# Performance work log

Measured on AMD Instinct MI355X. Metric: run time of the kernel, lower is better.

The kernel has to match this reference:

```python
import jax, jax.numpy as jnp
import numpy as np

DIM = 256
HEADS = 8
WIN = 8
HIDDEN = 1024
EPS = 1e-5

def _rel_pos_index(w):
    coords = np.stack(np.meshgrid(np.arange(w), np.arange(w), indexing='ij'))  # [2,w,w]
    cf = coords.reshape(2, -1)
    rel = cf[:, :, None] - cf[:, None, :]  # [2,N,N]
    rel = rel.transpose(1, 2, 0)
    rel[:, :, 0] += w - 1
    rel[:, :, 1] += w - 1
    rel[:, :, 0] *= 2 * w - 1
    return jnp.asarray(rel.sum(-1))  # [N,N] int

REL_IDX = _rel_pos_index(WIN)

def _layernorm(x, g, b):
    mu = jnp.mean(x, -1, keepdims=True)
    var = jnp.mean(jnp.square(x - mu), -1, keepdims=True)
    return (x - mu) * jax.lax.rsqrt(var + EPS) * g + b

def setup_inputs() -> dict:
    key = jax.random.key(0)
    ks = jax.random.split(key, 12)
    s = 0.02
    return {
        'x': jax.random.normal(ks[0], (16, 4096, 256), jnp.float32),
        'H': 64,
        'W': 64,
        'ln1_g': jnp.ones((DIM,), jnp.float32),
        'ln1_b': jnp.zeros((DIM,), jnp.float32),
        'qkv_w': jax.random.normal(ks[1], (DIM, 3 * DIM), jnp.float32) * s,
        'proj_w': jax.random.normal(ks[2], (DIM, DIM), jnp.float32) * s,
        'proj_b': jnp.zeros((DIM,), jnp.float32),
        'rel_bias_table': jax.random.normal(ks[3], ((2 * WIN - 1) ** 2, HEADS), jnp.float32) * s,
        'ln2_g': jnp.ones((DIM,), jnp.float32),
        'ln2_b': jnp.zeros((DIM,), jnp.float32),
        'fc1_w': jax.random.normal(ks[4], (DIM, HIDDEN), jnp.float32) * s,
        'fc1_b': jnp.zeros((HIDDEN,), jnp.float32),
        'fc2_w': jax.random.normal(ks[5], (HIDDEN, DIM), jnp.float32) * s,
        'fc2_b': jnp.zeros((DIM,), jnp.float32),
    }

def reference(x, H, W, ln1_g, ln1_b, qkv_w, proj_w, proj_b, rel_bias_table,
              ln2_g, ln2_b, fc1_w, fc1_b, fc2_w, fc2_b):
    B, L, C = x.shape
    w = WIN
    N = w * w
    head_dim = C // HEADS
    scale = head_dim ** -0.5

    shortcut = x
    h = _layernorm(x, ln1_g, ln1_b).reshape(B, H, W, C)
    # H, W chosen divisible by window_size -> pad_h = pad_w = 0 (faithful fast path)
    # window partition: [B*nW, N, C]
    h = h.reshape(B, H // w, w, W // w, w, C).transpose(0, 1, 3, 2, 4, 5)
    xw = h.reshape(-1, N, C)
    Bw = xw.shape[0]

    qkv = (xw @ qkv_w).reshape(Bw, N, 3, HEADS, head_dim)
    q = qkv[:, :, 0].transpose(0, 2, 1, 3) * scale  # [Bw,h,N,d]
    k = qkv[:, :, 1].transpose(0, 2, 1, 3)
    v = qkv[:, :, 2].transpose(0, 2, 1, 3)

    attn = jnp.einsum('bhnd,bhmd->bhnm', q, k)
    bias = rel_bias_table[REL_IDX.reshape(-1)].reshape(N, N, HEADS).transpose(2, 0, 1)
    attn = jax.nn.softmax(attn + bias[None], axis=-1)
    out = jnp.einsum('bhnm,bhmd->bhnd', attn, v).transpose(0, 2, 1, 3).reshape(Bw, N, C)
    out = out @ proj_w + proj_b

    # window reverse
    out = out.reshape(B, H // w, W // w, w, w, C).transpose(0, 1, 3, 2, 4, 5)
    out = out.reshape(B, L, C)

    x = shortcut + out
    h2 = _layernorm(x, ln2_g, ln2_b)
    mlp = jax.nn.gelu(h2 @ fc1_w + fc1_b, approximate=False) @ fc2_w + fc2_b
    return x + mlp
```

## Files before the change

kernel.cpp:

```cpp
#include <hip/hip_runtime.h>
#include <hip/hip_bf16.h>

typedef __attribute__((ext_vector_type(8))) short bf16x8;
typedef __attribute__((ext_vector_type(4))) float f32x4;

typedef __attribute__((address_space(3))) void LdsVoid;
typedef const __attribute__((address_space(1))) void GblVoid;

__device__ __forceinline__ void gload16(const void* g, void* l) {
  __builtin_amdgcn_global_load_lds((GblVoid*)g, (LdsVoid*)l, 16, 0, 0);
}

__device__ __forceinline__ unsigned short f2bf(float f) {
  union { float f; unsigned int u; } x; x.f = f;
  unsigned int r = (x.u + 0x7fffu + ((x.u >> 16) & 1u)) >> 16;
  return (unsigned short)r;
}

__global__ __launch_bounds__(256) void prep_w(
    const float* __restrict__ qw, const float* __restrict__ pw,
    const float* __restrict__ f1, const float* __restrict__ f2,
    unsigned short* __restrict__ out) {
  int idx = blockIdx.x * 256 + threadIdx.x;
  if (idx < 196608) { int n = idx >> 8, k = idx & 255; out[idx] = f2bf(qw[k * 768 + n]); return; }
  int i2 = idx - 196608;
  if (i2 < 65536) { int n = i2 >> 8, k = i2 & 255; out[idx] = f2bf(pw[k * 256 + n]); return; }
  int i3 = i2 - 65536;
  if (i3 < 262144) { int n = i3 >> 8, k = i3 & 255; out[idx] = f2bf(f1[k * 1024 + n]); return; }
  int i4 = i3 - 262144;
  { int n = i4 >> 10, k = i4 & 1023; out[idx] = f2bf(f2[k * 256 + n]); }
}

__global__ __launch_bounds__(256) void ln1_kernel(
    const float* __restrict__ x, const float* __restrict__ g, const float* __restrict__ b,
    unsigned short* __restrict__ xn) {
  int lane = threadIdx.x & 63, wid = threadIdx.x >> 6;
  size_t t = (size_t)blockIdx.x * 4 + wid;
  float4 v = ((const float4*)(x + t * 256))[lane];
  float s = v.x + v.y + v.z + v.w;
  #pragma unroll
  for (int m = 1; m < 64; m <<= 1) s += __shfl_xor(s, m);
  float mean = s * (1.0f / 256.0f);
  float dx = v.x - mean, dy = v.y - mean, dz = v.z - mean, dw = v.w - mean;
  float q = dx * dx + dy * dy + dz * dz + dw * dw;
  #pragma unroll
  for (int m = 1; m < 64; m <<= 1) q += __shfl_xor(q, m);
  float rstd = rsqrtf(q * (1.0f / 256.0f) + 1e-5f);
  float4 gg = ((const float4*)g)[lane];
  float4 bb = ((const float4*)b)[lane];
  unsigned int o0 = f2bf(dx * rstd * gg.x + bb.x) | ((unsigned int)f2bf(dy * rstd * gg.y + bb.y) << 16);
  unsigned int o1 = f2bf(dz * rstd * gg.z + bb.z) | ((unsigned int)f2bf(dw * rstd * gg.w + bb.w) << 16);
  int bI = (int)(t >> 12), rem = (int)t & 4095, y = rem >> 6, xc = rem & 63;
  size_t r = ((size_t)(bI * 64 + (y >> 3) * 8 + (xc >> 3))) * 64 + (y & 7) * 8 + (xc & 7);
  uint2 o; o.x = o0; o.y = o1;
  ((uint2*)(xn + r * 256))[lane] = o;
}

template <int EPI>
__global__ __launch_bounds__(256) void gemm_bt(
    const unsigned short* __restrict__ A, const unsigned short* __restrict__ Bt,
    unsigned short* __restrict__ outb, float* __restrict__ outf,
    const float* __restrict__ bias, int M, int N, int K) {
  __shared__ __align__(16) unsigned short lds_a[128 * 32];
  __shared__ __align__(16) unsigned short lds_b[128 * 32];
  const int tid = threadIdx.x;
  const int lane = tid & 63, wid = tid >> 6;
  const int cl = lane & 15, cg = lane >> 4;
  const size_t m0 = (size_t)blockIdx.y * 128;
  const size_t n0 = (size_t)blockIdx.x * 128;
  const int wr = wid >> 1, wc = wid & 1;
  f32x4 acc[4][4] = {};

  const unsigned short* aptr = A + (m0 + (tid >> 2)) * K + (tid & 3) * 8;
  const unsigned short* bptr = Bt + (n0 + (tid >> 2)) * K + (tid & 3) * 8;
  unsigned short* la = lds_a + wid * 512;
  unsigned short* lb = lds_b + wid * 512;
  const size_t astep = (size_t)64 * K;

  for (int k0 = 0; k0 < K; k0 += 32) {
    __syncthreads();
    gload16(aptr + k0, la);
    gload16(aptr + astep + k0, la + 2048);
    gload16(bptr + k0, lb);
    gload16(bptr + astep + k0, lb + 2048);
    __syncthreads();
    bf16x8 af[4], bfr[4];
    const unsigned short* pa = lds_a + (wr * 64 + cl) * 32 + cg * 8;
    const unsigned short* pb = lds_b + (wc * 64 + cl) * 32 + cg * 8;
    #pragma unroll
    for (int i = 0; i < 4; ++i) af[i] = *(const bf16x8*)(pa + i * 512);
    #pragma unroll
    for (int i = 0; i < 4; ++i) bfr[i] = *(const bf16x8*)(pb + i * 512);
    #pragma unroll
    for (int mi = 0; mi < 4; ++mi)
      #pragma unroll
      for (int ni = 0; ni < 4; ++ni)
        acc[mi][ni] = __builtin_amdgcn_mfma_f32_16x16x32_bf16(af[mi], bfr[ni], acc[mi][ni], 0, 0, 0);
  }

  #pragma unroll
  for (int mi = 0; mi < 4; ++mi) {
    #pragma unroll
    for (int ni = 0; ni < 4; ++ni) {
      #pragma unroll
      for (int r = 0; r < 4; ++r) {
        size_t row = m0 + wr * 64 + mi * 16 + cg * 4 + r;
        size_t col = n0 + wc * 64 + ni * 16 + cl;
        float v = acc[mi][ni][r];
        if (EPI == 0) {
          outb[row * N + col] = f2bf(v);
        } else if (EPI == 1) {
          float t = v + bias[col];
          outb[row * N + col] = f2bf(0.5f * t * (1.0f + erff(t * 0.70710678118654752f)));
        } else if (EPI == 2) {
          outf[row * N + col] = v + bias[col];
        } else {
          outf[row * N + col] += v + bias[col];
        }
      }
    }
  }
}

__global__ __launch_bounds__(256) void attn_win(
    const unsigned short* __restrict__ qkv, const float* __restrict__ table,
    unsigned short* __restrict__ out) {
  __shared__ float tbl[1800];
  __shared__ __align__(16) unsigned short p_lds[4][64 * 72];
  __shared__ __align__(16) unsigned short vt_lds[4][32 * 72];
  const int tid = threadIdx.x, lane = tid & 63, wid = tid >> 6;
  const int cl = lane & 15, cg = lane >> 4;
  for (int i = tid; i < 1800; i += 256) tbl[i] = table[i];
  __syncthreads();
  const size_t wbase = (size_t)blockIdx.x * 64;
  unsigned short* P = p_lds[wid];
  unsigned short* VT = vt_lds[wid];
  const float scale = 0.17677669529663687f;

  for (int hh = 0; hh < 2; ++hh) {
    const int h = wid + hh * 4;
    const int qoff = h * 32, koff = 256 + h * 32, voff = 512 + h * 32;
    bf16x8 qf[4], kf[4];
    #pragma unroll
    for (int mi = 0; mi < 4; ++mi)
      qf[mi] = *(const bf16x8*)&qkv[(wbase + mi * 16 + cl) * 768 + qoff + cg * 8];
    #pragma unroll
    for (int nj = 0; nj < 4; ++nj)
      kf[nj] = *(const bf16x8*)&qkv[(wbase + nj * 16 + cl) * 768 + koff + cg * 8];
    f32x4 S[4][4] = {};
    #pragma unroll
    for (int mi = 0; mi < 4; ++mi)
      #pragma unroll
      for (int nj = 0; nj < 4; ++nj)
        S[mi][nj] = __builtin_amdgcn_mfma_f32_16x16x32_bf16(qf[mi], kf[nj], S[mi][nj], 0, 0, 0);

    {
      const unsigned short* vrow = &qkv[(wbase + lane) * 768 + voff];
      unsigned short tmp[32];
      #pragma unroll
      for (int p = 0; p < 4; ++p) *(uint4*)&tmp[p * 8] = ((const uint4*)vrow)[p];
      #pragma unroll
      for (int d = 0; d < 32; ++d) VT[d * 72 + lane] = tmp[d];
    }

    float rs[4][4];
    #pragma unroll
    for (int mi = 0; mi < 4; ++mi) {
      #pragma unroll
      for (int r = 0; r < 4; ++r) {
        const int i = mi * 16 + cg * 4 + r;
        const int yi = i >> 3, xi = i & 7;
        float v[4];
        float m = -1e30f;
        #pragma unroll
        for (int nj = 0; nj < 4; ++nj) {
          const int j = nj * 16 + cl;
          const int yj = j >> 3, xj = j & 7;
          float bia = tbl[((yi - yj + 7) * 15 + (xi - xj + 7)) * 8 + h];
          v[nj] = S[mi][nj][r] * scale + bia;
          m = fmaxf(m, v[nj]);
        }
        #pragma unroll
        for (int mk = 1; mk < 16; mk <<= 1) m = fmaxf(m, __shfl_xor(m, mk));
        float s = 0.0f;
        #pragma unroll
        for (int nj = 0; nj < 4; ++nj) { v[nj] = expf(v[nj] - m); s += v[nj]; }
        #pragma unroll
        for (int mk = 1; mk < 16; mk <<= 1) s += __shfl_xor(s, mk);
        rs[mi][r] = s;
        #pragma unroll
        for (int nj = 0; nj < 4; ++nj) P[i * 72 + nj * 16 + cl] = f2bf(v[nj]);
      }
    }

    f32x4 O[4][2] = {};
    #pragma unroll
    for (int ks = 0; ks < 2; ++ks) {
      bf16x8 pa[4], vb[2];
      #pragma unroll
      for (int mi = 0; mi < 4; ++mi)
        pa[mi] = *(const bf16x8*)&P[(mi * 16 + cl) * 72 + ks * 32 + cg * 8];
      #pragma unroll
      for (int nd = 0; nd < 2; ++nd)
        vb[nd] = *(const bf16x8*)&VT[(nd * 16 + cl) * 72 + ks * 32 + cg * 8];
      #pragma unroll
      for (int mi = 0; mi < 4; ++mi)
        #pragma unroll
        for (int nd = 0; nd < 2; ++nd)
          O[mi][nd] = __builtin_amdgcn_mfma_f32_16x16x32_bf16(pa[mi], vb[nd], O[mi][nd], 0, 0, 0);
    }

    #pragma unroll
    for (int mi = 0; mi < 4; ++mi)
      #pragma unroll
      for (int nd = 0; nd < 2; ++nd)
        #pragma unroll
        for (int r = 0; r < 4; ++r) {
          float val = O[mi][nd][r] / rs[mi][r];
          out[(wbase + mi * 16 + cg * 4 + r) * 256 + h * 32 + nd * 16 + cl] = f2bf(val);
        }
  }
}

__global__ __launch_bounds__(256) void ep1_kernel(
    const float* __restrict__ x, const float* __restrict__ pout,
    const float* __restrict__ g, const float* __restrict__ b,
    float* __restrict__ x2out, unsigned short* __restrict__ h2) {
  int lane = threadIdx.x & 63, wid = threadIdx.x >> 6;
  size_t t = (size_t)blockIdx.x * 4 + wid;
  int bI = (int)(t >> 12), rem = (int)t & 4095, y = rem >> 6, xc = rem & 63;
  size_t r = ((size_t)(bI * 64 + (y >> 3) * 8 + (xc >> 3))) * 64 + (y & 7) * 8 + (xc & 7);
  float4 xv = ((const float4*)(x + t * 256))[lane];
  float4 pv = ((const float4*)(pout + r * 256))[lane];
  float4 s4; s4.x = xv.x + pv.x; s4.y = xv.y + pv.y; s4.z = xv.z + pv.z; s4.w = xv.w + pv.w;
  ((float4*)(x2out + t * 256))[lane] = s4;
  float s = s4.x + s4.y + s4.z + s4.w;
  #pragma unroll
  for (int m = 1; m < 64; m <<= 1) s += __shfl_xor(s, m);
  float mean = s * (1.0f / 256.0f);
  float dx = s4.x - mean, dy = s4.y - mean, dz = s4.z - mean, dw = s4.w - mean;
  float q = dx * dx + dy * dy + dz * dz + dw * dw;
  #pragma unroll
  for (int m = 1; m < 64; m <<= 1) q += __shfl_xor(q, m);
  float rstd = rsqrtf(q * (1.0f / 256.0f) + 1e-5f);
  float4 gg = ((const float4*)g)[lane];
  float4 bb = ((const float4*)b)[lane];
  uint2 o;
  o.x = f2bf(dx * rstd * gg.x + bb.x) | ((unsigned int)f2bf(dy * rstd * gg.y + bb.y) << 16);
  o.y = f2bf(dz * rstd * gg.z + bb.z) | ((unsigned int)f2bf(dw * rstd * gg.w + bb.w) << 16);
  ((uint2*)(h2 + t * 256))[lane] = o;
}

extern "C" void kernel_launch(void* const* d_in, const int* in_sizes, int n_in,
                              void* d_out, int out_size, void* d_ws, size_t ws_size,
                              hipStream_t stream) {
  (void)in_sizes; (void)n_in; (void)out_size; (void)ws_size;
  const float* x       = (const float*)d_in[0];
  const float* ln1_g   = (const float*)d_in[3];
  const float* ln1_b   = (const float*)d_in[4];
  const float* qkv_w   = (const float*)d_in[5];
  const float* proj_w  = (const float*)d_in[6];
  const float* proj_b  = (const float*)d_in[7];
  const float* rel_tbl = (const float*)d_in[8];
  const float* ln2_g   = (const float*)d_in[9];
  const float* ln2_b   = (const float*)d_in[10];
  const float* fc1_w   = (const float*)d_in[11];
  const float* fc1_b   = (const float*)d_in[12];
  const float* fc2_w   = (const float*)d_in[13];
  const float* fc2_b   = (const float*)d_in[14];
  float* out = (float*)d_out;

  char* ws = (char*)d_ws;
  const size_t OFF_XN   = 1572864;
  const size_t OFF_QKV  = OFF_XN + 33554432;
  const size_t OFF_ATTN = OFF_QKV + 100663296;
  unsigned short* Wt      = (unsigned short*)ws;
  unsigned short* xn      = (unsigned short*)(ws + OFF_XN);
  unsigned short* h2      = xn;
  unsigned short* qkv     = (unsigned short*)(ws + OFF_QKV);
  float*          projout = (float*)(ws + OFF_QKV);
  unsigned short* fc1out  = (unsigned short*)(ws + OFF_QKV);
  unsigned short* attnout = (unsigned short*)(ws + OFF_ATTN);

  prep_w<<<3072, 256, 0, stream>>>(qkv_w, proj_w, fc1_w, fc2_w, Wt);
  ln1_kernel<<<16384, 256, 0, stream>>>(x, ln1_g, ln1_b, xn);
  gemm_bt<0><<<dim3(6, 512), 256, 0, stream>>>(xn, Wt, qkv, nullptr, nullptr, 65536, 768, 256);
  attn_win<<<1024, 256, 0, stream>>>(qkv, rel_tbl, attnout);
  gemm_bt<2><<<dim3(2, 512), 256, 0, stream>>>(attnout, Wt + 196608, nullptr, projout, proj_b, 65536, 256, 256);
  ep1_kernel<<<16384, 256, 0, stream>>>(x, projout, ln2_g, ln2_b, out, h2);
  gemm_bt<1><<<dim3(8, 512), 256, 0, stream>>>(h2, Wt + 262144, fc1out, nullptr, fc1_b, 65536, 1024, 256);
  gemm_bt<3><<<dim3(2, 512), 256, 0, stream>>>(fc1out, Wt + 524288, nullptr, out, fc2_b, 65536, 256, 1024);
}
```

Baseline: 519.1 us.

## Triple-buffer GEMM LDS tiles with async prefetch and XOR swizzle

```diff
diff --git a/kernel.cpp b/kernel.cpp
--- a/kernel.cpp
+++ b/kernel.cpp
@@ -61,8 +61,7 @@
     const unsigned short* __restrict__ A, const unsigned short* __restrict__ Bt,
     unsigned short* __restrict__ outb, float* __restrict__ outf,
     const float* __restrict__ bias, int M, int N, int K) {
-  __shared__ __align__(16) unsigned short lds_a[128 * 32];
-  __shared__ __align__(16) unsigned short lds_b[128 * 32];
+  __shared__ __align__(16) unsigned short lds[3 * 8192];
   const int tid = threadIdx.x;
   const int lane = tid & 63, wid = tid >> 6;
   const int cl = lane & 15, cg = lane >> 4;
@@ -71,32 +70,60 @@
   const int wr = wid >> 1, wc = wid & 1;
   f32x4 acc[4][4] = {};
 
-  const unsigned short* aptr = A + (m0 + (tid >> 2)) * K + (tid & 3) * 8;
-  const unsigned short* bptr = Bt + (n0 + (tid >> 2)) * K + (tid & 3) * 8;
-  unsigned short* la = lds_a + wid * 512;
-  unsigned short* lb = lds_b + wid * 512;
+  const int ra = tid >> 2;
+  const int sc = ((tid & 3) ^ (ra & 3)) * 8;
+  const unsigned short* aptr = A + (m0 + ra) * K + sc;
+  const unsigned short* bptr = Bt + (n0 + ra) * K + sc;
   const size_t astep = (size_t)64 * K;
-
-  for (int k0 = 0; k0 < K; k0 += 32) {
-    __syncthreads();
-    gload16(aptr + k0, la);
-    gload16(aptr + astep + k0, la + 2048);
-    gload16(bptr + k0, lb);
-    gload16(bptr + astep + k0, lb + 2048);
-    __syncthreads();
-    bf16x8 af[4], bfr[4];
-    const unsigned short* pa = lds_a + (wr * 64 + cl) * 32 + cg * 8;
-    const unsigned short* pb = lds_b + (wc * 64 + cl) * 32 + cg * 8;
-    #pragma unroll
-    for (int i = 0; i < 4; ++i) af[i] = *(const bf16x8*)(pa + i * 512);
-    #pragma unroll
-    for (int i = 0; i < 4; ++i) bfr[i] = *(const bf16x8*)(pb + i * 512);
-    #pragma unroll
-    for (int mi = 0; mi < 4; ++mi)
-      #pragma unroll
-      for (int ni = 0; ni < 4; ++ni)
-        acc[mi][ni] = __builtin_amdgcn_mfma_f32_16x16x32_bf16(af[mi], bfr[ni], acc[mi][ni], 0, 0, 0);
+  unsigned short* wbaseA = lds + wid * 512;
+  unsigned short* wbaseB = lds + 4096 + wid * 512;
+
+  const int nt = K >> 5;
+
+  #define STAGE(T, B)                                            \
+    {                                                            \
+      const unsigned short* as_ = aptr + (T) * 32;               \
+      const unsigned short* bs_ = bptr + (T) * 32;               \
+      unsigned short* da_ = wbaseA + (B) * 8192;                 \
+      unsigned short* db_ = wbaseB + (B) * 8192;                 \
+      gload16(as_, da_); gload16(as_ + astep, da_ + 2048);       \
+      gload16(bs_, db_); gload16(bs_ + astep, db_ + 2048);       \
+    }
+
+  const int rsw = (cg ^ (cl & 3)) * 8;
+
+  #define COMPUTE(B)                                                             \
+    {                                                                            \
+      const unsigned short* base_ = lds + (B) * 8192;                            \
+      bf16x8 af[4], bfr[4];                                                      \
+      _Pragma("unroll")                                                          \
+      for (int i = 0; i < 4; ++i)                                                \
+        af[i] = *(const bf16x8*)(base_ + (wr * 64 + i * 16 + cl) * 32 + rsw);    \
+      _Pragma("unroll")                                                          \
+      for (int i = 0; i < 4; ++i)                                                \
+        bfr[i] = *(const bf16x8*)(base_ + 4096 + (wc * 64 + i * 16 + cl) * 32 + rsw); \
+      _Pragma("unroll")                                                          \
+      for (int mi = 0; mi < 4; ++mi)                                             \
+        _Pragma("unroll")                                                        \
+        for (int ni = 0; ni < 4; ++ni)                                           \
+          acc[mi][ni] = __builtin_amdgcn_mfma_f32_16x16x32_bf16(af[mi], bfr[ni], acc[mi][ni], 0, 0, 0); \
+    }
+
+  STAGE(0, 0);
+  STAGE(1, 1);
+  int c0 = 0, c1 = 1, c2 = 2;
+  for (int t = 0; t < nt - 1; ++t) {
+    asm volatile("s_waitcnt vmcnt(4)" ::: "memory");
+    __builtin_amdgcn_s_barrier();
+    if (t + 2 < nt) STAGE(t + 2, c2);
+    COMPUTE(c0);
+    int tmp = c0; c0 = c1; c1 = c2; c2 = tmp;
   }
+  asm volatile("s_waitcnt vmcnt(0)" ::: "memory");
+  __builtin_amdgcn_s_barrier();
+  COMPUTE(c0);
+  #undef STAGE
+  #undef COMPUTE
 
   #pragma unroll
   for (int mi = 0; mi < 4; ++mi) {
```

New measurement: 489.6 us. -5.7%, faster.

## Double-buffer GEMM k-loop with swizzled LDS, remap blocks, fuse residual into proj epilogue

Applied to the files above, without the earlier changes.

```diff
diff --git a/kernel.cpp b/kernel.cpp
--- a/kernel.cpp
+++ b/kernel.cpp
@@ -60,43 +60,76 @@
 __global__ __launch_bounds__(256) void gemm_bt(
     const unsigned short* __restrict__ A, const unsigned short* __restrict__ Bt,
     unsigned short* __restrict__ outb, float* __restrict__ outf,
-    const float* __restrict__ bias, int M, int N, int K) {
-  __shared__ __align__(16) unsigned short lds_a[128 * 32];
-  __shared__ __align__(16) unsigned short lds_b[128 * 32];
+    const float* __restrict__ bias, const float* __restrict__ xres,
+    int M, int N, int K) {
+  __shared__ __align__(16) unsigned short lds[2 * 16384];
   const int tid = threadIdx.x;
   const int lane = tid & 63, wid = tid >> 6;
   const int cl = lane & 15, cg = lane >> 4;
-  const size_t m0 = (size_t)blockIdx.y * 128;
-  const size_t n0 = (size_t)blockIdx.x * 128;
+  const unsigned nwg = gridDim.x * gridDim.y;
+  const unsigned orig = blockIdx.y * gridDim.x + blockIdx.x;
+  const unsigned virt = (orig & 7) * (nwg >> 3) + (orig >> 3);
+  const unsigned bx = virt % gridDim.x, by = virt / gridDim.x;
+  const size_t m0 = (size_t)by * 128;
+  const size_t n0 = (size_t)bx * 128;
   const int wr = wid >> 1, wc = wid & 1;
   f32x4 acc[4][4] = {};
 
-  const unsigned short* aptr = A + (m0 + (tid >> 2)) * K + (tid & 3) * 8;
-  const unsigned short* bptr = Bt + (n0 + (tid >> 2)) * K + (tid & 3) * 8;
-  unsigned short* la = lds_a + wid * 512;
-  unsigned short* lb = lds_b + wid * 512;
-  const size_t astep = (size_t)64 * K;
-
-  for (int k0 = 0; k0 < K; k0 += 32) {
-    __syncthreads();
-    gload16(aptr + k0, la);
-    gload16(aptr + astep + k0, la + 2048);
-    gload16(bptr + k0, lb);
-    gload16(bptr + astep + k0, lb + 2048);
-    __syncthreads();
-    bf16x8 af[4], bfr[4];
-    const unsigned short* pa = lds_a + (wr * 64 + cl) * 32 + cg * 8;
-    const unsigned short* pb = lds_b + (wc * 64 + cl) * 32 + cg * 8;
-    #pragma unroll
-    for (int i = 0; i < 4; ++i) af[i] = *(const bf16x8*)(pa + i * 512);
-    #pragma unroll
-    for (int i = 0; i < 4; ++i) bfr[i] = *(const bf16x8*)(pb + i * 512);
-    #pragma unroll
-    for (int mi = 0; mi < 4; ++mi)
-      #pragma unroll
-      for (int ni = 0; ni < 4; ++ni)
-        acc[mi][ni] = __builtin_amdgcn_mfma_f32_16x16x32_bf16(af[mi], bfr[ni], acc[mi][ni], 0, 0, 0);
+  const int r8 = lane >> 3;
+  const int gsw = ((lane & 7) ^ r8) * 8;
+  const unsigned short* aStage = A + (m0 + wid * 32 + r8) * K + gsw;
+  const unsigned short* bStage = Bt + (n0 + wid * 32 + r8) * K + gsw;
+  const size_t jstep = (size_t)8 * K;
+  const int nt = K >> 6;
+
+  #define STAGE(T, B)                                                   \
+    { const int ko_ = (T) * 64;                                         \
+      unsigned short* la_ = lds + (B) * 16384 + wid * 2048;             \
+      unsigned short* lb_ = la_ + 8192;                                 \
+      _Pragma("unroll")                                                 \
+      for (int j = 0; j < 4; ++j) {                                     \
+        gload16(aStage + ko_ + j * jstep, la_ + j * 512);               \
+        gload16(bStage + ko_ + j * jstep, lb_ + j * 512);               \
+      } }
+
+  bf16x8 af[2][4], bfr[2][4];
+  #define READF(B)                                                          \
+    { const unsigned short* base_ = lds + (B) * 16384;                      \
+      _Pragma("unroll")                                                     \
+      for (int kk = 0; kk < 2; ++kk)                                        \
+        _Pragma("unroll")                                                   \
+        for (int i = 0; i < 4; ++i) {                                       \
+          const int sl_ = ((kk * 4 + cg) ^ (cl & 7)) * 8;                   \
+          af[kk][i]  = *(const bf16x8*)(base_ + (wr * 64 + i * 16 + cl) * 64 + sl_);        \
+          bfr[kk][i] = *(const bf16x8*)(base_ + 8192 + (wc * 64 + i * 16 + cl) * 64 + sl_); \
+        } }
+
+  #define MFMAS()                                                           \
+    { _Pragma("unroll")                                                     \
+      for (int kk = 0; kk < 2; ++kk)                                        \
+        _Pragma("unroll")                                                   \
+        for (int mi = 0; mi < 4; ++mi)                                      \
+          _Pragma("unroll")                                                 \
+          for (int ni = 0; ni < 4; ++ni)                                    \
+            acc[mi][ni] = __builtin_amdgcn_mfma_f32_16x16x32_bf16(af[kk][mi], bfr[kk][ni], acc[mi][ni], 0, 0, 0); }
+
+  STAGE(0, 0);
+  STAGE(1, 1);
+  for (int t = 0; t < nt; ++t) {
+    if (t == nt - 1) { asm volatile("s_waitcnt vmcnt(0)" ::: "memory"); }
+    else             { asm volatile("s_waitcnt vmcnt(8)" ::: "memory"); }
+    __builtin_amdgcn_s_barrier();
+    READF(t & 1);
+    __builtin_amdgcn_sched_barrier(0);
+    asm volatile("s_waitcnt lgkmcnt(0)" ::: "memory");
+    __builtin_amdgcn_s_barrier();
+    __builtin_amdgcn_sched_barrier(0);
+    if (t + 2 < nt) STAGE(t + 2, t & 1);
+    MFMAS();
   }
+  #undef STAGE
+  #undef READF
+  #undef MFMAS
 
   #pragma unroll
   for (int mi = 0; mi < 4; ++mi) {
@@ -112,10 +145,13 @@
         } else if (EPI == 1) {
           float t = v + bias[col];
           outb[row * N + col] = f2bf(0.5f * t * (1.0f + erff(t * 0.70710678118654752f)));
-        } else if (EPI == 2) {
-          outf[row * N + col] = v + bias[col];
-        } else {
+        } else if (EPI == 3) {
           outf[row * N + col] += v + bias[col];
+        } else if (EPI == 4) {
+          int winr = (int)(row >> 6), pos = (int)(row & 63);
+          int bI = winr >> 6, wy = (winr >> 3) & 7, wx = winr & 7;
+          size_t tt = (size_t)bI * 4096 + (size_t)(wy * 8 + (pos >> 3)) * 64 + wx * 8 + (pos & 7);
+          outf[tt * 256 + col] = v + bias[col] + xres[tt * 256 + col];
         }
       }
     }
@@ -222,23 +258,17 @@
   }
 }
 
-__global__ __launch_bounds__(256) void ep1_kernel(
-    const float* __restrict__ x, const float* __restrict__ pout,
-    const float* __restrict__ g, const float* __restrict__ b,
-    float* __restrict__ x2out, unsigned short* __restrict__ h2) {
+__global__ __launch_bounds__(256) void ln2_kernel(
+    const float* __restrict__ x2, const float* __restrict__ g, const float* __restrict__ b,
+    unsigned short* __restrict__ h2) {
   int lane = threadIdx.x & 63, wid = threadIdx.x >> 6;
   size_t t = (size_t)blockIdx.x * 4 + wid;
-  int bI = (int)(t >> 12), rem = (int)t & 4095, y = rem >> 6, xc = rem & 63;
-  size_t r = ((size_t)(bI * 64 + (y >> 3) * 8 + (xc >> 3))) * 64 + (y & 7) * 8 + (xc & 7);
-  float4 xv = ((const float4*)(x + t * 256))[lane];
-  float4 pv = ((const float4*)(pout + r * 256))[lane];
-  float4 s4; s4.x = xv.x + pv.x; s4.y = xv.y + pv.y; s4.z = xv.z + pv.z; s4.w = xv.w + pv.w;
-  ((float4*)(x2out + t * 256))[lane] = s4;
-  float s = s4.x + s4.y + s4.z + s4.w;
+  float4 v = ((const float4*)(x2 + t * 256))[lane];
+  float s = v.x + v.y + v.z + v.w;
   #pragma unroll
   for (int m = 1; m < 64; m <<= 1) s += __shfl_xor(s, m);
   float mean = s * (1.0f / 256.0f);
-  float dx = s4.x - mean, dy = s4.y - mean, dz = s4.z - mean, dw = s4.w - mean;
+  float dx = v.x - mean, dy = v.y - mean, dz = v.z - mean, dw = v.w - mean;
   float q = dx * dx + dy * dy + dz * dz + dw * dw;
   #pragma unroll
   for (int m = 1; m < 64; m <<= 1) q += __shfl_xor(q, m);
@@ -278,16 +308,15 @@
   unsigned short* xn      = (unsigned short*)(ws + OFF_XN);
   unsigned short* h2      = xn;
   unsigned short* qkv     = (unsigned short*)(ws + OFF_QKV);
-  float*          projout = (float*)(ws + OFF_QKV);
   unsigned short* fc1out  = (unsigned short*)(ws + OFF_QKV);
   unsigned short* attnout = (unsigned short*)(ws + OFF_ATTN);
 
   prep_w<<<3072, 256, 0, stream>>>(qkv_w, proj_w, fc1_w, fc2_w, Wt);
   ln1_kernel<<<16384, 256, 0, stream>>>(x, ln1_g, ln1_b, xn);
-  gemm_bt<0><<<dim3(6, 512), 256, 0, stream>>>(xn, Wt, qkv, nullptr, nullptr, 65536, 768, 256);
+  gemm_bt<0><<<dim3(6, 512), 256, 0, stream>>>(xn, Wt, qkv, nullptr, nullptr, nullptr, 65536, 768, 256);
   attn_win<<<1024, 256, 0, stream>>>(qkv, rel_tbl, attnout);
-  gemm_bt<2><<<dim3(2, 512), 256, 0, stream>>>(attnout, Wt + 196608, nullptr, projout, proj_b, 65536, 256, 256);
-  ep1_kernel<<<16384, 256, 0, stream>>>(x, projout, ln2_g, ln2_b, out, h2);
-  gemm_bt<1><<<dim3(8, 512), 256, 0, stream>>>(h2, Wt + 262144, fc1out, nullptr, fc1_b, 65536, 1024, 256);
-  gemm_bt<3><<<dim3(2, 512), 256, 0, stream>>>(fc1out, Wt + 524288, nullptr, out, fc2_b, 65536, 256, 1024);
-}
+  gemm_bt<4><<<dim3(2, 512), 256, 0, stream>>>(attnout, Wt + 196608, nullptr, out, proj_b, x, 65536, 256, 256);
+  ln2_kernel<<<16384, 256, 0, stream>>>(out, ln2_g, ln2_b, h2);
+  gemm_bt<1><<<dim3(8, 512), 256, 0, stream>>>(h2, Wt + 262144, fc1out, nullptr, fc1_b, nullptr, 65536, 1024, 256);
+  gemm_bt<3><<<dim3(2, 512), 256, 0, stream>>>(fc1out, Wt + 524288, nullptr, out, fc2_b, nullptr, 65536, 256, 1024);
+}
```

Measured after the change: 455.3 us. 12.3% less time.
